# Kernel tuning notes

Measured on AMD Instinct MI355X. Metric: run time of the kernel, lower is better.

The kernel has to match this reference:

```python
import jax, jax.numpy as jnp
import numpy as np

N = 50000      # query points
M = 50000      # support points
H = 32         # max neighbors
K = 15         # kernel points
CIN = 64
COUT = 128
KP_EXTENT = 0.06
RADIUS = 0.05


def setup_inputs() -> dict:
    key = jax.random.key(0)
    k1, k2, k3, k4, k5, k6, k7 = jax.random.split(key, 7)
    # point coordinates in a small cube so neighbors fall within KP_extent of kernel points
    q_pts = jax.random.uniform(k1, (N, 3), dtype=jnp.float32) * 0.1
    s_pts = jax.random.uniform(k2, (M, 3), dtype=jnp.float32) * 0.1
    # indices in [0, M]; index M selects the shadow (padded) support point
    neighb_inds = jax.random.randint(k3, (N, H), 0, M + 1)
    x = jax.random.normal(k4, (M, CIN), dtype=jnp.float32)
    # kaiming-uniform-like init for [K, Cin, Cout] weights
    weights = jax.random.normal(k5, (K, CIN, COUT), dtype=jnp.float32) / np.sqrt(CIN)
    # kernel points uniformly in a sphere of radius RADIUS, center point fixed at origin
    d = jax.random.normal(k6, (K, 3), dtype=jnp.float32)
    d = d / jnp.linalg.norm(d, axis=1, keepdims=True)
    r = jax.random.uniform(k7, (K, 1), dtype=jnp.float32) ** (1.0 / 3.0) * RADIUS
    kernel_points = (d * r).at[0].set(0.0)
    return {"q_pts": q_pts, "s_pts": s_pts, "x": x, "weights": weights,
            "kernel_points": kernel_points, "neighb_inds": neighb_inds}


def reference(q_pts, s_pts, x, weights, kernel_points, neighb_inds):
    # pad support points with a far-away shadow point (matches torch: +1e6)
    s_pad = jnp.concatenate([s_pts, jnp.full((1, s_pts.shape[1]), 1e6, s_pts.dtype)], axis=0)
    # gather neighbor coords and center on queries: [N, H, 3]
    neighbors = s_pad[neighb_inds] - q_pts[:, None, :]
    # squared distances to each kernel point: [N, H, K]
    diff = neighbors[:, :, None, :] - kernel_points[None, None, :, :]
    sq_d = jnp.sum(diff * diff, axis=3)
    # linear influence, transposed to [N, K, H]
    h = jnp.maximum(1.0 - jnp.sqrt(sq_d) / KP_EXTENT, 0.0)
    h = jnp.swapaxes(h, 1, 2)
    # pad features with a zero row for shadow neighbors, then gather: [N, H, Cin]
    x_pad = jnp.concatenate([x, jnp.zeros((1, x.shape[1]), x.dtype)], axis=0)
    neighb_x = x_pad[neighb_inds]
    # project features onto kernel points: [N, K, Cin]
    fpk = jnp.einsum('nkh,nhc->nkc', h, neighb_x)
    # per-kernel-point matmul + sum over kernel points: [N, Cout]
    out = jnp.einsum('nkc,kco->no', fpk, weights)
    return out
```

## Files before the change

### kernel.cpp

```cpp
#include <hip/hip_runtime.h>

#define NQ     50000
#define MS     50000
#define NH     32
#define NK     15
#define CIN    64
#define COUT   128
#define QT     32
#define INV_EXT (1.0f/0.06f)

typedef unsigned int   uint32;
typedef unsigned short u16;
typedef _Float16 f16;
typedef _Float16 f16x8 __attribute__((ext_vector_type(8)));
typedef float    f32x4 __attribute__((ext_vector_type(4)));

#define WB_BYTES  (8*32*64*8*2)
#define XPH_BYTES (MS*CIN*2)

#if __has_builtin(__builtin_amdgcn_sqrtf)
#define SQRTF __builtin_amdgcn_sqrtf
#else
#define SQRTF sqrtf
#endif

__device__ __forceinline__ uint32 permlo(uint32 A, uint32 B) {
#if __has_builtin(__builtin_amdgcn_perm)
    return __builtin_amdgcn_perm(A, B, 0x01000504u);
#else
    return (A & 0xffffu) | (B << 16);
#endif
}
__device__ __forceinline__ uint32 permhi(uint32 A, uint32 B) {
#if __has_builtin(__builtin_amdgcn_perm)
    return __builtin_amdgcn_perm(A, B, 0x03020706u);
#else
    return (A >> 16) | (B & 0xffff0000u);
#endif
}

__device__ __forceinline__ u16 f16bits(float f) {
    return __builtin_bit_cast(u16, (f16)f);
}

__device__ __forceinline__ uint32 pk2(float a, float b) {
#if __has_builtin(__builtin_amdgcn_cvt_pkrtz)
    return __builtin_bit_cast(uint32, __builtin_amdgcn_cvt_pkrtz(a, b));
#else
    return (uint32)f16bits(a) | ((uint32)f16bits(b) << 16);
#endif
}


__global__ __launch_bounds__(256)
void pack_all(const float* __restrict__ x, u16* __restrict__ xph,
              const float* __restrict__ w, u16* __restrict__ wb) {
    const int bid = blockIdx.x;
    if (bid < 3125) {
        const int tid = bid * 256 + threadIdx.x;
        const int row = tid >> 4;
        const int lp  = tid & 15;
        const float v0 = x[row*CIN +  0 + lp];
        const float v1 = x[row*CIN + 16 + lp];
        const float v2 = x[row*CIN + 32 + lp];
        const float v3 = x[row*CIN + 48 + lp];
        uint2 d;
        d.x = pk2(v0, v1);
        d.y = pk2(v2, v3);
        *(uint2*)&xph[row*CIN + lp*4] = d;
    } else {
        const int u  = (bid - 3125) * 4 + (threadIdx.x >> 6);
        const int nt = u >> 5;
        const int ks = u & 31;
        const int l  = threadIdx.x & 63;
        u16 frag[8];
        #pragma unroll
        for (int e = 0; e < 8; ++e) {
            const int Kp = ks*32 + (l >> 4)*8 + e;
            const int c  = Kp >> 4;
            const int k  = Kp & 15;
            const float val = (k < NK) ? w[(k*CIN + c)*COUT + nt*16 + (l & 15)] : 0.0f;
            frag[e] = f16bits(val);
        }
        *(f16x8*)&wb[((nt*32 + ks)*64 + l)*8] = *(f16x8*)frag;
    }
}

__global__ __launch_bounds__(512, 4)
void kpconv_fused(const float* __restrict__ q_pts,
                  const float* __restrict__ s_pts,
                  const u16*  __restrict__ xph,
                  const u16*  __restrict__ wb,
                  const float* __restrict__ kp,
                  const int*   __restrict__ nind,
                  float* __restrict__ out)
{
    __shared__ u16   fpkAT[QT*1024];
    __shared__ float nb[QT*100];
    __shared__ u16   inds[QT*NH];

    const int t  = threadIdx.x;
    const int q0 = blockIdx.x * QT;

    #pragma unroll
    for (int p = t; p < QT*NH; p += 512) {
        const int q = p >> 5, j = p & 31;
        const int qg = q0 + q;
        const int qc = (qg < NQ) ? qg : (NQ - 1);
        const int ind = nind[qc*NH + j];
        const bool valid = (ind < MS);
        inds[p] = (u16)(valid ? ind : 0);
        float sx, sy, sz;
        if (valid) { sx = s_pts[ind*3+0]; sy = s_pts[ind*3+1]; sz = s_pts[ind*3+2]; }
        else       { sx = 1e6f; sy = 1e6f; sz = 1e6f; }
        nb[q*100 + j*3 + 0] = sx - q_pts[qc*3+0];
        nb[q*100 + j*3 + 1] = sy - q_pts[qc*3+1];
        nb[q*100 + j*3 + 2] = sz - q_pts[qc*3+2];
    }
    __syncthreads();

    {
        const int l  = t & 63, wv = t >> 6;
        const int lc = l & 15, lg = l >> 4;
        const int kc = (lc < NK) ? lc : (NK - 1);
        const float kx = kp[kc*3+0], ky = kp[kc*3+1], kz = kp[kc*3+2];
        const uint32 lcxor = (uint32)(lc & 4) << 2;

        uint2 v[4][8];
        #pragma unroll
        for (int qi = 0; qi < 4; ++qi) {
            const int q = wv*4 + qi;
            const uint4 iv = *(const uint4*)&inds[q*NH + lg*8];
            uint32 r[8];
            r[0] = iv.x & 0xffffu; r[1] = iv.x >> 16;
            r[2] = iv.y & 0xffffu; r[3] = iv.y >> 16;
            r[4] = iv.z & 0xffffu; r[5] = iv.z >> 16;
            r[6] = iv.w & 0xffffu; r[7] = iv.w >> 16;
            #pragma unroll
            for (int e = 0; e < 8; ++e)
                v[qi][e] = *(const uint2*)(xph + r[e]*CIN + lc*4);
        }
        __builtin_amdgcn_sched_barrier(0);

        #pragma unroll
        for (int qi = 0; qi < 4; ++qi) {
            const int q = wv*4 + qi;
            const float* nbq = &nb[q*100 + lg*24];
            const float4 r0 = *(const float4*)(nbq +  0);
            const float4 r1 = *(const float4*)(nbq +  4);
            const float4 r2 = *(const float4*)(nbq +  8);
            const float4 r3 = *(const float4*)(nbq + 12);
            const float4 r4 = *(const float4*)(nbq + 16);
            const float4 r5 = *(const float4*)(nbq + 20);
            float jx[8], jy[8], jz[8];
            jx[0]=r0.x; jy[0]=r0.y; jz[0]=r0.z;
            jx[1]=r0.w; jy[1]=r1.x; jz[1]=r1.y;
            jx[2]=r1.z; jy[2]=r1.w; jz[2]=r2.x;
            jx[3]=r2.y; jy[3]=r2.z; jz[3]=r2.w;
            jx[4]=r3.x; jy[4]=r3.y; jz[4]=r3.z;
            jx[5]=r3.w; jy[5]=r4.x; jz[5]=r4.y;
            jx[6]=r4.z; jy[6]=r4.w; jz[6]=r5.x;
            jx[7]=r5.y; jy[7]=r5.z; jz[7]=r5.w;
            float hh[8];
            #pragma unroll
            for (int e = 0; e < 8; ++e) {
                const float dx = jx[e] - kx;
                const float dy = jy[e] - ky;
                const float dz = jz[e] - kz;
                float h = 1.0f - SQRTF(dx*dx + dy*dy + dz*dz) * INV_EXT;
                hh[e] = (h > 0.0f) ? h : 0.0f;
            }
            uint32 ab[4];
            ab[0] = pk2(hh[0], hh[1]); ab[1] = pk2(hh[2], hh[3]);
            ab[2] = pk2(hh[4], hh[5]); ab[3] = pk2(hh[6], hh[7]);
            const f16x8 a = __builtin_bit_cast(f16x8, *(uint4*)ab);
            f32x4 acc0 = {0,0,0,0}, acc1 = {0,0,0,0}, acc2 = {0,0,0,0}, acc3 = {0,0,0,0};
            #pragma unroll
            for (int ct = 0; ct < 4; ++ct) {
                const uint32 A0 = (ct & 2) ? v[qi][0].y : v[qi][0].x, B0 = (ct & 2) ? v[qi][1].y : v[qi][1].x;
                const uint32 A1 = (ct & 2) ? v[qi][2].y : v[qi][2].x, B1 = (ct & 2) ? v[qi][3].y : v[qi][3].x;
                const uint32 A2 = (ct & 2) ? v[qi][4].y : v[qi][4].x, B2 = (ct & 2) ? v[qi][5].y : v[qi][5].x;
                const uint32 A3 = (ct & 2) ? v[qi][6].y : v[qi][6].x, B3 = (ct & 2) ? v[qi][7].y : v[qi][7].x;
                uint4 bd;
                if (ct & 1) {
                    bd.x = permhi(A0, B0); bd.y = permhi(A1, B1);
                    bd.z = permhi(A2, B2); bd.w = permhi(A3, B3);
                } else {
                    bd.x = permlo(A0, B0); bd.y = permlo(A1, B1);
                    bd.z = permlo(A2, B2); bd.w = permlo(A3, B3);
                }
                const f16x8 b = __builtin_bit_cast(f16x8, bd);
                if      (ct == 0) acc0 = __builtin_amdgcn_mfma_f32_16x16x32_f16(a, b, acc0, 0,0,0);
                else if (ct == 1) acc1 = __builtin_amdgcn_mfma_f32_16x16x32_f16(a, b, acc1, 0,0,0);
                else if (ct == 2) acc2 = __builtin_amdgcn_mfma_f32_16x16x32_f16(a, b, acc2, 0,0,0);
                else              acc3 = __builtin_amdgcn_mfma_f32_16x16x32_f16(a, b, acc3, 0,0,0);
            }
            {
                const uint32 wbase = ((uint32)(q*2048 + lc*32 + lg*8))
                                     ^ (((uint32)(q & 7)) << 4) ^ lcxor;
                char* wp = (char*)fpkAT + wbase;
                #pragma unroll
                for (int ct = 0; ct < 4; ++ct) {
                    const f32x4 av = (ct==0)?acc0:(ct==1)?acc1:(ct==2)?acc2:acc3;
                    uint2 dv;
                    dv.x = pk2(av[0], av[1]);
                    dv.y = pk2(av[2], av[3]);
                    *(uint2*)(wp + ct*512) = dv;
                }
            }
        }
    }

    const int l  = t & 63;
    const int nt = t >> 6;
    const u16* bp = wb + (nt*32)*512 + l*8;
    uint4 bufA[8], bufB[8];
    #pragma unroll
    for (int e = 0; e < 8; ++e) bufA[e] = *(const uint4*)(bp + e*512);

    __syncthreads();

    {
        const int col = l & 15;
        const int kg  = l >> 4;
        f32x4 acc0 = {0.f,0.f,0.f,0.f};
        f32x4 acc1 = {0.f,0.f,0.f,0.f};
        const uint32 b0 = ((uint32)(col*2048 + kg*16)) ^ (((uint32)(col & 7)) << 4);
        const char* base = (const char*)fpkAT;
        const char* p0 = base + (b0);
        const char* p1 = base + (b0 ^ 64u);
        const char* p2 = base + (b0 ^ 144u);
        const char* p3 = base + (b0 ^ 208u);

#define PROC(G, BUF)                                                              \
        _Pragma("unroll")                                                         \
        for (int e = 0; e < 8; ++e) {                                             \
            const int ks = (G)*8 + e;                                             \
            const char* sel = ((ks & 3) == 0) ? p0 : ((ks & 3) == 1) ? p1         \
                            : ((ks & 3) == 2) ? p2 : p3;                          \
            const int off = (ks >> 2) * 256;                                      \
            const f16x8 a0 = *(const f16x8*)(sel + off);                          \
            const f16x8 a1 = *(const f16x8*)(sel + off + 32768);                  \
            const f16x8 b  = __builtin_bit_cast(f16x8, BUF[e]);                   \
            acc0 = __builtin_amdgcn_mfma_f32_16x16x32_f16(a0, b, acc0, 0, 0, 0);  \
            acc1 = __builtin_amdgcn_mfma_f32_16x16x32_f16(a1, b, acc1, 0, 0, 0);  \
        }

        #pragma unroll
        for (int e = 0; e < 8; ++e) bufB[e] = *(const uint4*)(bp + (8 + e)*512);
        __builtin_amdgcn_sched_barrier(0);
        PROC(0, bufA)
        #pragma unroll
        for (int e = 0; e < 8; ++e) bufA[e] = *(const uint4*)(bp + (16 + e)*512);
        __builtin_amdgcn_sched_barrier(0);
        PROC(1, bufB)
        #pragma unroll
        for (int e = 0; e < 8; ++e) bufB[e] = *(const uint4*)(bp + (24 + e)*512);
        __builtin_amdgcn_sched_barrier(0);
        PROC(2, bufA)
        PROC(3, bufB)
#undef PROC

        const int rbase = kg * 4;
        #pragma unroll
        for (int r = 0; r < 4; ++r) {
            const int row0 = q0 + rbase + r;
            const int row1 = row0 + 16;
            if (row0 < NQ) out[row0*COUT + nt*16 + col] = acc0[r];
            if (row1 < NQ) out[row1*COUT + nt*16 + col] = acc1[r];
        }
    }
}

extern "C" void kernel_launch(void* const* d_in, const int* in_sizes, int n_in,
                              void* d_out, int out_size, void* d_ws, size_t ws_size,
                              hipStream_t stream) {
    const float* q_pts = (const float*)d_in[0];
    const float* s_pts = (const float*)d_in[1];
    const float* x     = (const float*)d_in[2];
    const float* wts   = (const float*)d_in[3];
    const float* kp    = (const float*)d_in[4];
    const int*   nind  = (const int*)d_in[5];
    float* out = (float*)d_out;

    u16* wbp = (u16*)d_ws;
    u16* xph = (u16*)((char*)d_ws + WB_BYTES);

    hipLaunchKernelGGL(pack_all, dim3(3125 + 64), dim3(256), 0, stream, x, xph, wts, wbp);
    hipLaunchKernelGGL(kpconv_fused, dim3((NQ + QT - 1) / QT), dim3(512), 0, stream,
                       q_pts, s_pts, xph, wbp, kp, nind, out);
}
```

Before: 60.42 us.

## Hand-schedule gather and weight loads with inline asm and explicit vmcnt waits

The neighbor-feature gather now runs in two halves of two queries each, using inline-asm global loads. The h computation overlaps the in-flight loads, and one explicit vmcnt(0) wait precedes the MFMAs. The weight double-buffer in the second matmul also uses asm loads with counted vmcnt waits, and its first prefetch moves from before the barrier to after it. This lowers register pressure (16 gathered values live instead of 32) and controls latency hiding explicitly. The costs are less memory-level parallelism per wave, the loss of weight prefetch across the barrier, and asm volatile loads the compiler cannot reorder.

```diff
diff --git a/kernel.cpp b/kernel.cpp
--- a/kernel.cpp
+++ b/kernel.cpp
@@ -50,6 +50,19 @@
     return (uint32)f16bits(a) | ((uint32)f16bits(b) << 16);
 #endif
 }
+
+__device__ __forceinline__ uint2 ld_b64(const void* p) {
+    uint2 r;
+    asm volatile("global_load_dwordx2 %0, %1, off" : "=v"(r) : "v"(p));
+    return r;
+}
+__device__ __forceinline__ uint4 ld_b128(const void* p) {
+    uint4 r;
+    asm volatile("global_load_dwordx4 %0, %1, off" : "=v"(r) : "v"(p));
+    return r;
+}
+#define WAIT_VM(n) do { asm volatile("s_waitcnt vmcnt(" #n ")"); \
+                        __builtin_amdgcn_sched_barrier(0); } while (0)
 
 
 __global__ __launch_bounds__(256)
@@ -126,76 +139,96 @@
         const float kx = kp[kc*3+0], ky = kp[kc*3+1], kz = kp[kc*3+2];
         const uint32 lcxor = (uint32)(lc & 4) << 2;
 
-        uint2 v[4][8];
-        #pragma unroll
-        for (int qi = 0; qi < 4; ++qi) {
-            const int q = wv*4 + qi;
-            const uint4 iv = *(const uint4*)&inds[q*NH + lg*8];
-            uint32 r[8];
-            r[0] = iv.x & 0xffffu; r[1] = iv.x >> 16;
-            r[2] = iv.y & 0xffffu; r[3] = iv.y >> 16;
-            r[4] = iv.z & 0xffffu; r[5] = iv.z >> 16;
-            r[6] = iv.w & 0xffffu; r[7] = iv.w >> 16;
-            #pragma unroll
-            for (int e = 0; e < 8; ++e)
-                v[qi][e] = *(const uint2*)(xph + r[e]*CIN + lc*4);
-        }
-        __builtin_amdgcn_sched_barrier(0);
-
-        #pragma unroll
-        for (int qi = 0; qi < 4; ++qi) {
-            const int q = wv*4 + qi;
-            const float* nbq = &nb[q*100 + lg*24];
-            const float4 r0 = *(const float4*)(nbq +  0);
-            const float4 r1 = *(const float4*)(nbq +  4);
-            const float4 r2 = *(const float4*)(nbq +  8);
-            const float4 r3 = *(const float4*)(nbq + 12);
-            const float4 r4 = *(const float4*)(nbq + 16);
-            const float4 r5 = *(const float4*)(nbq + 20);
-            float jx[8], jy[8], jz[8];
-            jx[0]=r0.x; jy[0]=r0.y; jz[0]=r0.z;
-            jx[1]=r0.w; jy[1]=r1.x; jz[1]=r1.y;
-            jx[2]=r1.z; jy[2]=r1.w; jz[2]=r2.x;
-            jx[3]=r2.y; jy[3]=r2.z; jz[3]=r2.w;
-            jx[4]=r3.x; jy[4]=r3.y; jz[4]=r3.z;
-            jx[5]=r3.w; jy[5]=r4.x; jz[5]=r4.y;
-            jx[6]=r4.z; jy[6]=r4.w; jz[6]=r5.x;
-            jx[7]=r5.y; jy[7]=r5.z; jz[7]=r5.w;
-            float hh[8];
-            #pragma unroll
-            for (int e = 0; e < 8; ++e) {
-                const float dx = jx[e] - kx;
-                const float dy = jy[e] - ky;
-                const float dz = jz[e] - kz;
-                float h = 1.0f - SQRTF(dx*dx + dy*dy + dz*dz) * INV_EXT;
-                hh[e] = (h > 0.0f) ? h : 0.0f;
-            }
-            uint32 ab[4];
-            ab[0] = pk2(hh[0], hh[1]); ab[1] = pk2(hh[2], hh[3]);
-            ab[2] = pk2(hh[4], hh[5]); ab[3] = pk2(hh[6], hh[7]);
-            const f16x8 a = __builtin_bit_cast(f16x8, *(uint4*)ab);
-            f32x4 acc0 = {0,0,0,0}, acc1 = {0,0,0,0}, acc2 = {0,0,0,0}, acc3 = {0,0,0,0};
-            #pragma unroll
-            for (int ct = 0; ct < 4; ++ct) {
-                const uint32 A0 = (ct & 2) ? v[qi][0].y : v[qi][0].x, B0 = (ct & 2) ? v[qi][1].y : v[qi][1].x;
-                const uint32 A1 = (ct & 2) ? v[qi][2].y : v[qi][2].x, B1 = (ct & 2) ? v[qi][3].y : v[qi][3].x;
-                const uint32 A2 = (ct & 2) ? v[qi][4].y : v[qi][4].x, B2 = (ct & 2) ? v[qi][5].y : v[qi][5].x;
-                const uint32 A3 = (ct & 2) ? v[qi][6].y : v[qi][6].x, B3 = (ct & 2) ? v[qi][7].y : v[qi][7].x;
-                uint4 bd;
-                if (ct & 1) {
-                    bd.x = permhi(A0, B0); bd.y = permhi(A1, B1);
-                    bd.z = permhi(A2, B2); bd.w = permhi(A3, B3);
-                } else {
-                    bd.x = permlo(A0, B0); bd.y = permlo(A1, B1);
-                    bd.z = permlo(A2, B2); bd.w = permlo(A3, B3);
-                }
-                const f16x8 b = __builtin_bit_cast(f16x8, bd);
-                if      (ct == 0) acc0 = __builtin_amdgcn_mfma_f32_16x16x32_f16(a, b, acc0, 0,0,0);
-                else if (ct == 1) acc1 = __builtin_amdgcn_mfma_f32_16x16x32_f16(a, b, acc1, 0,0,0);
-                else if (ct == 2) acc2 = __builtin_amdgcn_mfma_f32_16x16x32_f16(a, b, acc2, 0,0,0);
-                else              acc3 = __builtin_amdgcn_mfma_f32_16x16x32_f16(a, b, acc3, 0,0,0);
+        #pragma unroll
+        for (int half = 0; half < 2; ++half) {
+            const int qA = wv*4 + half*2;
+            const int qB = qA + 1;
+
+            uint2 vA[8], vB[8];
+            {
+                const uint4 iv = *(const uint4*)&inds[qA*NH + lg*8];
+                uint32 r[8];
+                r[0] = iv.x & 0xffffu; r[1] = iv.x >> 16;
+                r[2] = iv.y & 0xffffu; r[3] = iv.y >> 16;
+                r[4] = iv.z & 0xffffu; r[5] = iv.z >> 16;
+                r[6] = iv.w & 0xffffu; r[7] = iv.w >> 16;
+                #pragma unroll
+                for (int e = 0; e < 8; ++e) vA[e] = ld_b64(xph + r[e]*CIN + lc*4);
             }
             {
+                const uint4 iv = *(const uint4*)&inds[qB*NH + lg*8];
+                uint32 r[8];
+                r[0] = iv.x & 0xffffu; r[1] = iv.x >> 16;
+                r[2] = iv.y & 0xffffu; r[3] = iv.y >> 16;
+                r[4] = iv.z & 0xffffu; r[5] = iv.z >> 16;
+                r[6] = iv.w & 0xffffu; r[7] = iv.w >> 16;
+                #pragma unroll
+                for (int e = 0; e < 8; ++e) vB[e] = ld_b64(xph + r[e]*CIN + lc*4);
+            }
+
+            f16x8 aF[2];
+            #pragma unroll
+            for (int s = 0; s < 2; ++s) {
+                const int q = qA + s;
+                const float* nbq = &nb[q*100 + lg*24];
+                const float4 r0 = *(const float4*)(nbq +  0);
+                const float4 r1 = *(const float4*)(nbq +  4);
+                const float4 r2 = *(const float4*)(nbq +  8);
+                const float4 r3 = *(const float4*)(nbq + 12);
+                const float4 r4 = *(const float4*)(nbq + 16);
+                const float4 r5 = *(const float4*)(nbq + 20);
+                float jx[8], jy[8], jz[8];
+                jx[0]=r0.x; jy[0]=r0.y; jz[0]=r0.z;
+                jx[1]=r0.w; jy[1]=r1.x; jz[1]=r1.y;
+                jx[2]=r1.z; jy[2]=r1.w; jz[2]=r2.x;
+                jx[3]=r2.y; jy[3]=r2.z; jz[3]=r2.w;
+                jx[4]=r3.x; jy[4]=r3.y; jz[4]=r3.z;
+                jx[5]=r3.w; jy[5]=r4.x; jz[5]=r4.y;
+                jx[6]=r4.z; jy[6]=r4.w; jz[6]=r5.x;
+                jx[7]=r5.y; jy[7]=r5.z; jz[7]=r5.w;
+                float hh[8];
+                #pragma unroll
+                for (int e = 0; e < 8; ++e) {
+                    const float dx = jx[e] - kx;
+                    const float dy = jy[e] - ky;
+                    const float dz = jz[e] - kz;
+                    float h = 1.0f - SQRTF(dx*dx + dy*dy + dz*dz) * INV_EXT;
+                    hh[e] = (h > 0.0f) ? h : 0.0f;
+                }
+                uint32 ab[4];
+                ab[0] = pk2(hh[0], hh[1]); ab[1] = pk2(hh[2], hh[3]);
+                ab[2] = pk2(hh[4], hh[5]); ab[3] = pk2(hh[6], hh[7]);
+                aF[s] = __builtin_bit_cast(f16x8, *(uint4*)ab);
+            }
+
+            WAIT_VM(0);
+
+            #pragma unroll
+            for (int s = 0; s < 2; ++s) {
+                const int q = qA + s;
+                const uint2* v = s ? vB : vA;
+                const f16x8 a = aF[s];
+                f32x4 acc0 = {0,0,0,0}, acc1 = {0,0,0,0}, acc2 = {0,0,0,0}, acc3 = {0,0,0,0};
+                #pragma unroll
+                for (int ct = 0; ct < 4; ++ct) {
+                    const uint32 A0 = (ct & 2) ? v[0].y : v[0].x, B0 = (ct & 2) ? v[1].y : v[1].x;
+                    const uint32 A1 = (ct & 2) ? v[2].y : v[2].x, B1 = (ct & 2) ? v[3].y : v[3].x;
+                    const uint32 A2 = (ct & 2) ? v[4].y : v[4].x, B2 = (ct & 2) ? v[5].y : v[5].x;
+                    const uint32 A3 = (ct & 2) ? v[6].y : v[6].x, B3 = (ct & 2) ? v[7].y : v[7].x;
+                    uint4 bd;
+                    if (ct & 1) {
+                        bd.x = permhi(A0, B0); bd.y = permhi(A1, B1);
+                        bd.z = permhi(A2, B2); bd.w = permhi(A3, B3);
+                    } else {
+                        bd.x = permlo(A0, B0); bd.y = permlo(A1, B1);
+                        bd.z = permlo(A2, B2); bd.w = permlo(A3, B3);
+                    }
+                    const f16x8 b = __builtin_bit_cast(f16x8, bd);
+                    if      (ct == 0) acc0 = __builtin_amdgcn_mfma_f32_16x16x32_f16(a, b, acc0, 0,0,0);
+                    else if (ct == 1) acc1 = __builtin_amdgcn_mfma_f32_16x16x32_f16(a, b, acc1, 0,0,0);
+                    else if (ct == 2) acc2 = __builtin_amdgcn_mfma_f32_16x16x32_f16(a, b, acc2, 0,0,0);
+                    else              acc3 = __builtin_amdgcn_mfma_f32_16x16x32_f16(a, b, acc3, 0,0,0);
+                }
                 const uint32 wbase = ((uint32)(q*2048 + lc*32 + lg*8))
                                      ^ (((uint32)(q & 7)) << 4) ^ lcxor;
                 char* wp = (char*)fpkAT + wbase;
@@ -214,9 +247,6 @@
     const int l  = t & 63;
     const int nt = t >> 6;
     const u16* bp = wb + (nt*32)*512 + l*8;
-    uint4 bufA[8], bufB[8];
-    #pragma unroll
-    for (int e = 0; e < 8; ++e) bufA[e] = *(const uint4*)(bp + e*512);
 
     __syncthreads();
 
@@ -231,6 +261,12 @@
         const char* p1 = base + (b0 ^ 64u);
         const char* p2 = base + (b0 ^ 144u);
         const char* p3 = base + (b0 ^ 208u);
+
+        uint4 bufA[8], bufB[8];
+        #pragma unroll
+        for (int e = 0; e < 8; ++e) bufA[e] = ld_b128(bp + e*512);
+        #pragma unroll
+        for (int e = 0; e < 8; ++e) bufB[e] = ld_b128(bp + (8+e)*512);
 
 #define PROC(G, BUF)                                                              \
         _Pragma("unroll")                                                         \
@@ -246,18 +282,17 @@
             acc1 = __builtin_amdgcn_mfma_f32_16x16x32_f16(a1, b, acc1, 0, 0, 0);  \
         }
 
-        #pragma unroll
-        for (int e = 0; e < 8; ++e) bufB[e] = *(const uint4*)(bp + (8 + e)*512);
-        __builtin_amdgcn_sched_barrier(0);
+        WAIT_VM(8);
         PROC(0, bufA)
         #pragma unroll
-        for (int e = 0; e < 8; ++e) bufA[e] = *(const uint4*)(bp + (16 + e)*512);
-        __builtin_amdgcn_sched_barrier(0);
+        for (int e = 0; e < 8; ++e) bufA[e] = ld_b128(bp + (16+e)*512);
+        WAIT_VM(8);
         PROC(1, bufB)
         #pragma unroll
-        for (int e = 0; e < 8; ++e) bufB[e] = *(const uint4*)(bp + (24 + e)*512);
-        __builtin_amdgcn_sched_barrier(0);
+        for (int e = 0; e < 8; ++e) bufB[e] = ld_b128(bp + (24+e)*512);
+        WAIT_VM(8);
         PROC(2, bufA)
+        WAIT_VM(0);
         PROC(3, bufB)
 #undef PROC
 
```

Result: no change. 60.65 us (+0.4%).
